# Optimization experiments

Measured on AMD Instinct MI355X. Metric: run time of the kernel, lower is better.

The kernel has to match this reference:

```python
import jax, jax.numpy as jnp
import numpy as np

VOCAB, EMB = 50000, 300
HID, FCH = 128, 64
B, T = 1024, 200


def setup_inputs() -> dict:
    key = jax.random.key(0)
    ks = jax.random.split(key, 10)
    s = 0.05
    return {
        "x": jax.random.randint(ks[0], (B, T), 0, VOCAB),
        "emb_table": jax.random.normal(ks[1], (VOCAB, EMB), jnp.float32) * s,
        "w_ih": jax.random.normal(ks[2], (4 * HID, EMB), jnp.float32) * s,
        "w_hh": jax.random.normal(ks[3], (4 * HID, HID), jnp.float32) * s,
        "b_ih": jax.random.normal(ks[4], (4 * HID,), jnp.float32) * s,
        "b_hh": jax.random.normal(ks[5], (4 * HID,), jnp.float32) * s,
        "fc1_w": jax.random.normal(ks[6], (FCH, HID), jnp.float32) * s,
        "fc1_b": jax.random.normal(ks[7], (FCH,), jnp.float32) * s,
        "fc2_w": jax.random.normal(ks[8], (1, FCH), jnp.float32) * s,
        "fc2_b": jax.random.normal(ks[9], (1,), jnp.float32) * s,
    }


def _lstm_last_h(e, w_ih, w_hh, b_ih, b_hh):
    # e: [B, T, E] -> final hidden state [B, H]
    b, t, _ = e.shape
    h_dim = w_hh.shape[1]
    # Precompute input projections for all timesteps: [T, B, 4H]
    xg = jnp.einsum('bte,ge->tbg', e, w_ih) + (b_ih + b_hh)

    def step(carry, xg_t):
        h, c = carry
        gates = xg_t + h @ w_hh.T  # [B, 4H]
        i, f, g, o = jnp.split(gates, 4, axis=-1)  # PyTorch gate order i,f,g,o
        i = jax.nn.sigmoid(i)
        f = jax.nn.sigmoid(f)
        g = jnp.tanh(g)
        o = jax.nn.sigmoid(o)
        c = f * c + i * g
        h = o * jnp.tanh(c)
        return (h, c), None

    h0 = jnp.zeros((b, h_dim), e.dtype)
    c0 = jnp.zeros((b, h_dim), e.dtype)
    (h_n, _), _ = jax.lax.scan(step, (h0, c0), xg)
    return h_n


def reference(x, emb_table, w_ih, w_hh, b_ih, b_hh, fc1_w, fc1_b, fc2_w, fc2_b):
    e = emb_table[x]  # [B, T, E]
    hn = _lstm_last_h(e, w_ih, w_hh, b_ih, b_hh)  # [B, H]
    # dropout is identity in eval mode
    h1 = jax.nn.relu(hn @ fc1_w.T + fc1_b)  # [B, FCH]
    logits = h1 @ fc2_w.T + fc2_b  # [B, 1]
    return jax.nn.sigmoid(logits)
```

## Files before the change

kernel.cpp:

```cpp
#include <hip/hip_runtime.h>
#include <hip/hip_bf16.h>
#include <stdint.h>

#define VOCAB 50000
#define EMB   300
#define EMBP  320
#define HID   128
#define NGATE 512
#define BATCH 1024
#define SEQ   200
#define ROWS  4
#define L2E   1.4426950408889634f

typedef __attribute__((ext_vector_type(8))) short short8;
typedef __attribute__((ext_vector_type(4))) float f32x4;

#define AS1 __attribute__((address_space(1)))
#define AS3 __attribute__((address_space(3)))

static __device__ __forceinline__ void gload_lds16(const void* g, void* s) {
  __builtin_amdgcn_global_load_lds((const AS1 uint32_t*)g, (AS3 uint32_t*)s, 16, 0, 0);
}

static __device__ __forceinline__ unsigned short f2bf(float f) {
  union { float f; unsigned u; } v; v.f = f;
  unsigned r = v.u + 0x7fffu + ((v.u >> 16) & 1u);
  return (unsigned short)(r >> 16);
}
static __device__ __forceinline__ float blo2f(unsigned u) {
  union { unsigned u; float f; } v; v.u = u << 16; return v.f;
}
static __device__ __forceinline__ float bhi2f(unsigned u) {
  union { unsigned u; float f; } v; v.u = u & 0xffff0000u; return v.f;
}
static __device__ __forceinline__ float sigmf(float x) {
  return __fdividef(1.0f, 1.0f + __expf(-x));
}
static __device__ __forceinline__ float sig2(float z) {
  return __builtin_amdgcn_rcpf(1.0f + __builtin_amdgcn_exp2f(-z));
}

__global__ void k_cvt_pad(const float* __restrict__ src, unsigned short* __restrict__ dst,
                          int rows, int sc, int dc, int perm, int smode) {
  int idx = blockIdx.x * blockDim.x + threadIdx.x;
  int cpr = dc >> 3;
  if (idx >= rows * cpr) return;
  int row = idx / cpr, k0 = (idx - row * cpr) * 8;
  float s = 1.0f;
  if (smode) s = ((row >> 7) == 2) ? (2.0f * L2E) : L2E;
  uint4 pack;
  unsigned short* v = (unsigned short*)&pack;
#pragma unroll
  for (int j = 0; j < 8; j++) {
    int k = k0 + j;
    v[j] = (k < sc) ? f2bf(src[(long)row * sc + k] * s) : (unsigned short)0;
  }
  int drow = perm ? ((row & 127) * 4 + (row >> 7)) : row;
  *(uint4*)(dst + (long)drow * dc + k0) = pack;
}

__global__ void k_bias(const float* __restrict__ a, const float* __restrict__ b,
                       float* __restrict__ o) {
  int i = blockIdx.x * blockDim.x + threadIdx.x;
  if (i < NGATE) {
    int g = i >> 7, hid = i & 127;
    float s = (g == 2) ? (2.0f * L2E) : L2E;
    o[hid * 4 + g] = (a[i] + b[i]) * s;
  }
}

__global__ __launch_bounds__(256) void k_xg_gemm(
    const int* __restrict__ x, const unsigned short* __restrict__ embb,
    const unsigned short* __restrict__ wihb, const float* __restrict__ biasp,
    unsigned short* __restrict__ xg) {
  __shared__ __align__(16) unsigned short Al[2][128 * 64];
  __shared__ __align__(16) unsigned short Bl[2][128 * 64];
  const int tid = threadIdx.x;
  const int lane = tid & 63;
  const int bid = blockIdx.x;
  const int xcd = bid & 7;
  const int q = bid >> 3;
  const int tile_m = xcd * 200 + (q >> 2);
  const int tile_n = q & 3;
  const int t_idx = tile_m >> 3;
  const int b0 = (tile_m & 7) * 128;
  const int n0 = tile_n * 128;

  const int r0 = tid >> 3;
  const int sg = (tid & 7) ^ (r0 & 7);
  const unsigned short* asrc[4];
  const unsigned short* bsrc[4];
#pragma unroll
  for (int i = 0; i < 4; i++) {
    const int r = r0 + i * 32;
    const long ridx = x[(b0 + r) * SEQ + t_idx];
    asrc[i] = embb + ridx * EMBP + sg * 8;
    bsrc[i] = wihb + (long)(n0 + r) * EMBP + sg * 8;
  }

  const int wid = tid >> 6;
  const int wrow = wid >> 1, wcol = wid & 1;
  const int l15 = lane & 15, lgrp = lane >> 4;
  const int swz = (l15 & 7) << 4;

  f32x4 acc[4][4];
#pragma unroll
  for (int mt = 0; mt < 4; mt++)
#pragma unroll
    for (int nt = 0; nt < 4; nt++) acc[mt][nt] = (f32x4){0.f, 0.f, 0.f, 0.f};

#define STAGE(KS, BUF)                                                         \
  {                                                                            \
    _Pragma("unroll") for (int i = 0; i < 4; i++) {                            \
      gload_lds16(asrc[i] + (KS) * 64, (char*)Al + (BUF) * 16384 + tid * 16 + i * 4096); \
      gload_lds16(bsrc[i] + (KS) * 64, (char*)Bl + (BUF) * 16384 + tid * 16 + i * 4096); \
    }                                                                          \
  }

#define COMPUTE(BUF)                                                           \
  {                                                                            \
    const char* Ar = (const char*)Al + (BUF) * 16384 + (wrow * 64) * 128;      \
    const char* Br = (const char*)Bl + (BUF) * 16384 + (wcol * 64) * 128;      \
    _Pragma("unroll") for (int kt = 0; kt < 2; kt++) {                         \
      short8 af[4], bf[4];                                                     \
      _Pragma("unroll") for (int mt = 0; mt < 4; mt++)                         \
        af[mt] = *(const short8*)(Ar + (mt * 16 + l15) * 128 + ((kt * 64 + lgrp * 16) ^ swz)); \
      _Pragma("unroll") for (int nt = 0; nt < 4; nt++)                         \
        bf[nt] = *(const short8*)(Br + (nt * 16 + l15) * 128 + ((kt * 64 + lgrp * 16) ^ swz)); \
      _Pragma("unroll") for (int mt = 0; mt < 4; mt++)                         \
        _Pragma("unroll") for (int nt = 0; nt < 4; nt++)                       \
          acc[mt][nt] = __builtin_amdgcn_mfma_f32_16x16x32_bf16(af[mt], bf[nt], acc[mt][nt], 0, 0, 0); \
    }                                                                          \
  }

  STAGE(0, 0);
  __syncthreads();
  STAGE(1, 1); COMPUTE(0); __syncthreads();
  STAGE(2, 0); COMPUTE(1); __syncthreads();
  STAGE(3, 1); COMPUTE(0); __syncthreads();
  STAGE(4, 0); COMPUTE(1); __syncthreads();
  COMPUTE(0);
#undef STAGE
#undef COMPUTE

  const int m_base = tile_m * 128 + wrow * 64;
  const int colg = n0 + wcol * 64 + l15;
  const int rsub = lgrp * 4;
  float bv[4];
#pragma unroll
  for (int nt = 0; nt < 4; nt++) bv[nt] = biasp[colg + nt * 16];
#pragma unroll
  for (int mt = 0; mt < 4; mt++)
#pragma unroll
    for (int nt = 0; nt < 4; nt++)
#pragma unroll
      for (int j = 0; j < 4; j++) {
        const long m = m_base + mt * 16 + rsub + j;
        xg[m * NGATE + colg + nt * 16] = f2bf(acc[mt][nt][j] + bv[nt]);
      }
}

__global__ __launch_bounds__(512, 2) void k_lstm(
    const unsigned short* __restrict__ xg, const unsigned short* __restrict__ whhp,
    float* __restrict__ hfin) {
  __shared__ __align__(16) unsigned short h_lds[2 * 4 * 128];
  __shared__ __align__(16) float scratch[8 * 256];
  const int tid = threadIdx.x;
  const int lane = tid & 63;
  const int wid = tid >> 6;
  const int b0 = blockIdx.x * ROWS;
  const int l15 = lane & 15;
  const int lgrp = lane >> 4;
  const int hid = wid * 16 + l15;

  short8 wfr[4][4];
#pragma unroll
  for (int nt = 0; nt < 4; nt++)
#pragma unroll
    for (int kt = 0; kt < 4; kt++)
      wfr[nt][kt] = *(const short8*)(whhp + (long)(wid * 64 + nt * 16 + l15) * HID + kt * 32 + lgrp * 8);

  float c_r = 0.0f, h_r = 0.0f;

  ((unsigned*)h_lds)[tid] = 0;
  __syncthreads();

  const int ar = l15 & 3;
  int rdoff[4];
#pragma unroll
  for (int kt = 0; kt < 4; kt++)
    rdoff[kt] = ar * 256 + ((kt * 64 + lgrp * 16) ^ (ar << 5));
  const int hwoff = lgrp * 256 + ((2 * hid) ^ (lgrp << 5));
  const char* lb = (const char*)h_lds;

  float* sw = scratch + wid * 256;
  int swr[4];
#pragma unroll
  for (int nt = 0; nt < 4; nt++)
    swr[nt] = l15 * 64 + (((nt * 4 + lgrp) * 4) ^ (l15 * 4));
  const int srd = lgrp * 64 + ((l15 * 4) ^ (lgrp * 4));

  const unsigned short* xbase = xg + ((long)(b0 + lgrp) * HID + hid) * 4;
  const long TSTEP = (long)BATCH * HID * 4;
  uint2 xA = *(const uint2*)xbase;
  uint2 xB = *(const uint2*)(xbase + TSTEP);
  const unsigned short* xnext = xbase + 2 * TSTEP;

#define STEP_BODY(XS, RB, WB, T)                                               \
  {                                                                            \
    const float xf0 = blo2f(XS.x), xf1 = bhi2f(XS.x);                          \
    const float xf2 = blo2f(XS.y), xf3 = bhi2f(XS.y);                          \
    if ((T) + 2 < SEQ) XS = *(const uint2*)xnext;                              \
    short8 hf[4];                                                              \
    _Pragma("unroll") for (int kt = 0; kt < 4; kt++)                           \
      hf[kt] = *(const short8*)(lb + (RB) + rdoff[kt]);                        \
    f32x4 acc[4];                                                              \
    _Pragma("unroll") for (int nt = 0; nt < 4; nt++)                           \
      acc[nt] = (f32x4){0.f, 0.f, 0.f, 0.f};                                   \
    _Pragma("unroll") for (int kt = 0; kt < 4; kt++)                           \
      _Pragma("unroll") for (int nt = 0; nt < 4; nt++)                         \
        acc[nt] = __builtin_amdgcn_mfma_f32_16x16x32_bf16(wfr[nt][kt], hf[kt], \
                                                          acc[nt], 0, 0, 0);   \
    if (l15 < 4) {                                                             \
      _Pragma("unroll") for (int nt = 0; nt < 4; nt++)                         \
        *(f32x4*)(sw + swr[nt]) = acc[nt];                                     \
    }                                                                          \
    asm volatile("s_waitcnt lgkmcnt(0)" ::: "memory");                         \
    const f32x4 g4 = *(const f32x4*)(sw + srd);                                \
    const float zi = g4[0] + xf0;                                              \
    const float zf = g4[1] + xf1;                                              \
    const float zg = g4[2] + xf2;                                              \
    const float zo = g4[3] + xf3;                                              \
    const float iv = sig2(zi);                                                 \
    const float fv = sig2(zf);                                                 \
    const float gv = 2.0f * sig2(zg) - 1.0f;                                   \
    const float ov = sig2(zo);                                                 \
    c_r = fv * c_r + iv * gv;                                                  \
    const float tc = 2.0f * sig2(c_r * (2.0f * L2E)) - 1.0f;                   \
    h_r = ov * tc;                                                             \
    *(unsigned short*)((char*)h_lds + (WB) + hwoff) = f2bf(h_r);               \
    asm volatile("s_waitcnt lgkmcnt(0)" ::: "memory");                         \
    __builtin_amdgcn_s_barrier();                                              \
    __builtin_amdgcn_sched_barrier(0);                                         \
  }

  for (int t = 0; t < SEQ; t += 2) {
    STEP_BODY(xA, 0, 1024, t);
    xnext += TSTEP;
    STEP_BODY(xB, 1024, 0, t + 1);
    xnext += TSTEP;
  }
#undef STEP_BODY

  hfin[(b0 + lgrp) * HID + hid] = h_r;
}

__global__ void k_head(const float* __restrict__ hfin,
                       const float* __restrict__ fc1w, const float* __restrict__ fc1b,
                       const float* __restrict__ fc2w, const float* __restrict__ fc2b,
                       float* __restrict__ out) {
  const int tid = threadIdx.x;
  const int lane = tid & 63;
  const int wid = tid >> 6;
  const int row = blockIdx.x * 4 + wid;
  const float* h = hfin + row * HID;
  const float* w = fc1w + lane * HID;
  float acc = 0.0f;
#pragma unroll
  for (int k = 0; k < HID; k += 4) {
    const f32x4 hv = *(const f32x4*)(h + k);
    const f32x4 wv = *(const f32x4*)(w + k);
    acc += hv[0] * wv[0] + hv[1] * wv[1] + hv[2] * wv[2] + hv[3] * wv[3];
  }
  const float h1 = fmaxf(acc + fc1b[lane], 0.0f);
  float v = h1 * fc2w[lane];
#pragma unroll
  for (int off = 32; off > 0; off >>= 1) v += __shfl_down(v, off, 64);
  if (lane == 0) out[row] = sigmf(v + fc2b[0]);
}

extern "C" void kernel_launch(void* const* d_in, const int* in_sizes, int n_in,
                              void* d_out, int out_size, void* d_ws, size_t ws_size,
                              hipStream_t stream) {
  const int*   x    = (const int*)d_in[0];
  const float* emb  = (const float*)d_in[1];
  const float* w_ih = (const float*)d_in[2];
  const float* w_hh = (const float*)d_in[3];
  const float* b_ih = (const float*)d_in[4];
  const float* b_hh = (const float*)d_in[5];
  const float* fc1w = (const float*)d_in[6];
  const float* fc1b = (const float*)d_in[7];
  const float* fc2w = (const float*)d_in[8];
  const float* fc2b = (const float*)d_in[9];
  float* out = (float*)d_out;
  char* ws = (char*)d_ws;

  unsigned short* embb = (unsigned short*)(ws + 0);
  unsigned short* wihb = (unsigned short*)(ws + 32000000);
  unsigned short* whhp = (unsigned short*)(ws + 32327680);
  float*          biasp= (float*)(ws + 32458752);
  float*          hfinp= (float*)(ws + 32460800);
  unsigned short* xgb  = (unsigned short*)(ws + 32985088);

  k_cvt_pad<<<dim3((VOCAB * (EMBP / 8) + 255) / 256), dim3(256), 0, stream>>>(emb, embb, VOCAB, EMB, EMBP, 0, 0);
  k_cvt_pad<<<dim3((NGATE * (EMBP / 8) + 255) / 256), dim3(256), 0, stream>>>(w_ih, wihb, NGATE, EMB, EMBP, 1, 1);
  k_cvt_pad<<<dim3((NGATE * (HID / 8) + 255) / 256), dim3(256), 0, stream>>>(w_hh, whhp, NGATE, HID, HID, 1, 1);
  k_bias<<<dim3(2), dim3(256), 0, stream>>>(b_ih, b_hh, biasp);
  k_xg_gemm<<<dim3(1600 * 4), dim3(256), 0, stream>>>(x, embb, wihb, biasp, xgb);
  k_lstm<<<dim3(BATCH / ROWS), dim3(512), 0, stream>>>(xgb, whhp, hfinp);
  k_head<<<dim3(256), dim3(256), 0, stream>>>(hfinp, fc1w, fc1b, fc2w, fc2b, out);
  (void)in_sizes; (void)n_in; (void)out_size; (void)ws_size;
}
```

Baseline: 289.7 us.

## Reuse gathered embedding tile across all gate columns in xg GEMM

```diff
diff --git a/kernel.cpp b/kernel.cpp
--- a/kernel.cpp
+++ b/kernel.cpp
@@ -69,95 +69,108 @@
   }
 }
 
-__global__ __launch_bounds__(256) void k_xg_gemm(
+__global__ __launch_bounds__(512, 1) void k_xg_gemm(
     const int* __restrict__ x, const unsigned short* __restrict__ embb,
     const unsigned short* __restrict__ wihb, const float* __restrict__ biasp,
     unsigned short* __restrict__ xg) {
-  __shared__ __align__(16) unsigned short Al[2][128 * 64];
+  __shared__ __align__(16) unsigned short Al[128 * EMBP];
   __shared__ __align__(16) unsigned short Bl[2][128 * 64];
   const int tid = threadIdx.x;
   const int lane = tid & 63;
-  const int bid = blockIdx.x;
-  const int xcd = bid & 7;
-  const int q = bid >> 3;
-  const int tile_m = xcd * 200 + (q >> 2);
-  const int tile_n = q & 3;
+  const int tile_m = blockIdx.x;
   const int t_idx = tile_m >> 3;
   const int b0 = (tile_m & 7) * 128;
-  const int n0 = tile_n * 128;
-
-  const int r0 = tid >> 3;
-  const int sg = (tid & 7) ^ (r0 & 7);
-  const unsigned short* asrc[4];
-  const unsigned short* bsrc[4];
-#pragma unroll
-  for (int i = 0; i < 4; i++) {
-    const int r = r0 + i * 32;
+
+#pragma unroll
+  for (int i = 0; i < 10; i++) {
+    const unsigned c = tid + i * 512;
+    const unsigned r = c / 40u;
+    const unsigned s = c - r * 40u;
+    const unsigned sg = s ^ (r & 7u);
     const long ridx = x[(b0 + r) * SEQ + t_idx];
-    asrc[i] = embb + ridx * EMBP + sg * 8;
-    bsrc[i] = wihb + (long)(n0 + r) * EMBP + sg * 8;
-  }
+    gload_lds16(embb + ridx * EMBP + sg * 8, (char*)Al + c * 16);
+  }
+  const unsigned bc0 = tid;
+  const unsigned br0 = bc0 >> 3, bp0 = bc0 & 7;
+  const unsigned bs0 = bp0 ^ (br0 & 7);
+  const unsigned bc1 = tid + 512;
+  const unsigned br1 = bc1 >> 3, bp1 = bc1 & 7;
+  const unsigned bs1 = bp1 ^ (br1 & 7);
+  gload_lds16(wihb + (long)br0 * EMBP + 0 * 64 + bs0 * 8, (char*)Bl + bc0 * 16);
+  gload_lds16(wihb + (long)br1 * EMBP + 0 * 64 + bs1 * 8, (char*)Bl + bc1 * 16);
+  __syncthreads();
 
   const int wid = tid >> 6;
   const int wrow = wid >> 1, wcol = wid & 1;
   const int l15 = lane & 15, lgrp = lane >> 4;
-  const int swz = (l15 & 7) << 4;
-
-  f32x4 acc[4][4];
-#pragma unroll
-  for (int mt = 0; mt < 4; mt++)
-#pragma unroll
-    for (int nt = 0; nt < 4; nt++) acc[mt][nt] = (f32x4){0.f, 0.f, 0.f, 0.f};
-
-#define STAGE(KS, BUF)                                                         \
-  {                                                                            \
-    _Pragma("unroll") for (int i = 0; i < 4; i++) {                            \
-      gload_lds16(asrc[i] + (KS) * 64, (char*)Al + (BUF) * 16384 + tid * 16 + i * 4096); \
-      gload_lds16(bsrc[i] + (KS) * 64, (char*)Bl + (BUF) * 16384 + tid * 16 + i * 4096); \
-    }                                                                          \
-  }
-
-#define COMPUTE(BUF)                                                           \
-  {                                                                            \
-    const char* Ar = (const char*)Al + (BUF) * 16384 + (wrow * 64) * 128;      \
-    const char* Br = (const char*)Bl + (BUF) * 16384 + (wcol * 64) * 128;      \
-    _Pragma("unroll") for (int kt = 0; kt < 2; kt++) {                         \
-      short8 af[4], bf[4];                                                     \
-      _Pragma("unroll") for (int mt = 0; mt < 4; mt++)                         \
-        af[mt] = *(const short8*)(Ar + (mt * 16 + l15) * 128 + ((kt * 64 + lgrp * 16) ^ swz)); \
-      _Pragma("unroll") for (int nt = 0; nt < 4; nt++)                         \
-        bf[nt] = *(const short8*)(Br + (nt * 16 + l15) * 128 + ((kt * 64 + lgrp * 16) ^ swz)); \
-      _Pragma("unroll") for (int mt = 0; mt < 4; mt++)                         \
-        _Pragma("unroll") for (int nt = 0; nt < 4; nt++)                       \
-          acc[mt][nt] = __builtin_amdgcn_mfma_f32_16x16x32_bf16(af[mt], bf[nt], acc[mt][nt], 0, 0, 0); \
-    }                                                                          \
-  }
-
-  STAGE(0, 0);
-  __syncthreads();
-  STAGE(1, 1); COMPUTE(0); __syncthreads();
-  STAGE(2, 0); COMPUTE(1); __syncthreads();
-  STAGE(3, 1); COMPUTE(0); __syncthreads();
-  STAGE(4, 0); COMPUTE(1); __syncthreads();
-  COMPUTE(0);
-#undef STAGE
-#undef COMPUTE
-
-  const int m_base = tile_m * 128 + wrow * 64;
-  const int colg = n0 + wcol * 64 + l15;
-  const int rsub = lgrp * 4;
-  float bv[4];
-#pragma unroll
-  for (int nt = 0; nt < 4; nt++) bv[nt] = biasp[colg + nt * 16];
-#pragma unroll
-  for (int mt = 0; mt < 4; mt++)
-#pragma unroll
-    for (int nt = 0; nt < 4; nt++)
-#pragma unroll
-      for (int j = 0; j < 4; j++) {
-        const long m = m_base + mt * 16 + rsub + j;
-        xg[m * NGATE + colg + nt * 16] = f2bf(acc[mt][nt][j] + bv[nt]);
+  const int swz7 = l15 & 7;
+
+  short8 af[2][10];
+#pragma unroll
+  for (int mt = 0; mt < 2; mt++) {
+    const int arow = wrow * 32 + mt * 16 + l15;
+    const char* abase = (const char*)Al + arow * (EMBP * 2);
+#pragma unroll
+    for (int kt = 0; kt < 10; kt++)
+      af[mt][kt] = *(const short8*)(abase + (((kt * 4 + lgrp) ^ swz7) << 4));
+  }
+
+  f32x4 acc[2][4];
+  const int brow_frag = wcol * 64;
+
+#pragma unroll
+  for (int n = 0; n < 4; n++) {
+    const int n0 = n * 128;
+    float bv[4];
+#pragma unroll
+    for (int nt = 0; nt < 4; nt++) bv[nt] = biasp[n0 + brow_frag + nt * 16 + l15];
+#pragma unroll
+    for (int mt = 0; mt < 2; mt++)
+#pragma unroll
+      for (int nt = 0; nt < 4; nt++) acc[mt][nt] = (f32x4){0.f, 0.f, 0.f, 0.f};
+
+#pragma unroll
+    for (int ckt = 0; ckt < 5; ckt++) {
+      const int cc = n * 5 + ckt;
+      if (cc < 19) {
+        const int n2 = (cc + 1) / 5, k2 = (cc + 1) % 5;
+        char* bbuf = (char*)Bl + ((cc + 1) & 1) * 16384;
+        gload_lds16(wihb + (long)(n2 * 128 + br0) * EMBP + k2 * 64 + bs0 * 8, bbuf + bc0 * 16);
+        gload_lds16(wihb + (long)(n2 * 128 + br1) * EMBP + k2 * 64 + bs1 * 8, bbuf + bc1 * 16);
       }
+      const char* bbase = (const char*)Bl + (cc & 1) * 16384;
+      short8 bf[4][2];
+#pragma unroll
+      for (int nt = 0; nt < 4; nt++) {
+        const int brow = brow_frag + nt * 16 + l15;
+        const char* bb = bbase + brow * 128;
+#pragma unroll
+        for (int kk = 0; kk < 2; kk++)
+          bf[nt][kk] = *(const short8*)(bb + (((kk * 4 + lgrp) ^ swz7) << 4));
+      }
+#pragma unroll
+      for (int kk = 0; kk < 2; kk++)
+#pragma unroll
+        for (int mt = 0; mt < 2; mt++)
+#pragma unroll
+          for (int nt = 0; nt < 4; nt++)
+            acc[mt][nt] = __builtin_amdgcn_mfma_f32_16x16x32_bf16(
+                af[mt][ckt * 2 + kk], bf[nt][kk], acc[mt][nt], 0, 0, 0);
+      __syncthreads();
+    }
+
+#pragma unroll
+    for (int mt = 0; mt < 2; mt++)
+#pragma unroll
+      for (int nt = 0; nt < 4; nt++) {
+        const int colg = n0 + brow_frag + nt * 16 + l15;
+#pragma unroll
+        for (int j = 0; j < 4; j++) {
+          const long m = (long)tile_m * 128 + wrow * 32 + mt * 16 + lgrp * 4 + j;
+          xg[m * NGATE + colg] = f2bf(acc[mt][nt][j] + bv[nt]);
+        }
+      }
+  }
 }
 
 __global__ __launch_bounds__(512, 2) void k_lstm(
@@ -225,7 +238,7 @@
       _Pragma("unroll") for (int nt = 0; nt < 4; nt++)                         \
         *(f32x4*)(sw + swr[nt]) = acc[nt];                                     \
     }                                                                          \
-    asm volatile("s_waitcnt lgkmcnt(0)" ::: "memory");                         \
+    __builtin_amdgcn_sched_barrier(0);                                         \
     const f32x4 g4 = *(const f32x4*)(sw + srd);                                \
     const float zi = g4[0] + xf0;                                              \
     const float zf = g4[1] + xf1;                                              \
@@ -306,7 +319,7 @@
   k_cvt_pad<<<dim3((NGATE * (EMBP / 8) + 255) / 256), dim3(256), 0, stream>>>(w_ih, wihb, NGATE, EMB, EMBP, 1, 1);
   k_cvt_pad<<<dim3((NGATE * (HID / 8) + 255) / 256), dim3(256), 0, stream>>>(w_hh, whhp, NGATE, HID, HID, 1, 1);
   k_bias<<<dim3(2), dim3(256), 0, stream>>>(b_ih, b_hh, biasp);
-  k_xg_gemm<<<dim3(1600 * 4), dim3(256), 0, stream>>>(x, embb, wihb, biasp, xgb);
+  k_xg_gemm<<<dim3(1600), dim3(512), 0, stream>>>(x, embb, wihb, biasp, xgb);
   k_lstm<<<dim3(BATCH / ROWS), dim3(512), 0, stream>>>(xgb, whhp, hfinp);
   k_head<<<dim3(256), dim3(256), 0, stream>>>(hfinp, fc1w, fc1b, fc2w, fc2b, out);
   (void)in_sizes; (void)n_in; (void)out_size; (void)ws_size;
```

Result: slower. 338.2 us (+16.7%).
